# Performance work log

Measured on AMD Instinct MI355X. Metric: run time of the kernel, lower is better.

Reference implementation:

```python
import jax, jax.numpy as jnp
import numpy as np

N = 100000
E = 1600000
IN_C, HID_C, OUT_C = 32, 64, 32


def setup_inputs() -> dict:
    key = jax.random.key(0)
    ks = jax.random.split(key, 10)
    x = jax.random.normal(ks[0], (N, IN_C), dtype=jnp.float32)
    edge_index = jax.random.randint(ks[1], (2, E), 0, N, dtype=jnp.int64)

    def lin(k, fan_in, fan_out):
        kw, kb = jax.random.split(k)
        bound = 1.0 / np.sqrt(fan_in)
        W = jax.random.uniform(kw, (fan_in, fan_out), minval=-bound, maxval=bound, dtype=jnp.float32)
        b = jax.random.uniform(kb, (fan_out,), minval=-bound, maxval=bound, dtype=jnp.float32)
        return W, b

    W1, b1 = lin(ks[2], IN_C, HID_C)
    W2, b2 = lin(ks[3], HID_C, HID_C)
    W3, b3 = lin(ks[4], HID_C, HID_C)
    W4, b4 = lin(ks[5], HID_C, OUT_C)
    return {"x": x, "edge_index": edge_index,
            "W1": W1, "b1": b1, "W2": W2, "b2": b2,
            "W3": W3, "b3": b3, "W4": W4, "b4": b4}


def _gin_conv(x, src, dst, W_a, b_a, W_b, b_b):
    # sum-aggregate neighbor features: messages x[src] scattered to dst
    agg = jax.ops.segment_sum(x[src], dst, num_segments=N)  # [N, d]
    h = agg + x  # (1 + eps) * x with eps = 0
    h = jax.nn.relu(h @ W_a + b_a)
    return h @ W_b + b_b


def reference(x, edge_index, W1, b1, W2, b2, W3, b3, W4, b4):
    src, dst = edge_index[0], edge_index[1]
    h = jax.nn.relu(_gin_conv(x, src, dst, W1, b1, W2, b2))
    out = _gin_conv(h, src, dst, W3, b3, W4, b4)
    return out
```

## Files before the change

kernel.cpp:

```cpp
#include <hip/hip_runtime.h>
#include <hip/hip_fp16.h>

#define NN 100000
#define NE 1600000
#define NB 391
#define NS 13
#define NSP1 14
#define SLICE_SHIFT 13
#define NSEG 391
#define EPB 4096
#define GRID_E 391

typedef _Float16 h2_t __attribute__((ext_vector_type(2)));

__device__ __forceinline__ unsigned pkh2(float lo, float hi) {
    auto v = __builtin_amdgcn_cvt_pkrtz(lo, hi);
    unsigned u; __builtin_memcpy(&u, &v, 4); return u;
}
__device__ __forceinline__ float fdot2u(unsigned a, unsigned b, float c) {
    h2_t x, y; __builtin_memcpy(&x, &a, 4); __builtin_memcpy(&y, &b, 4);
    return __builtin_amdgcn_fdot2(x, y, c, false);
}

__device__ __forceinline__ void h4acc(float2 raw, float& ax, float& ay, float& az, float& aw) {
    __half2 lo = *reinterpret_cast<__half2*>(&raw.x);
    __half2 hi = *reinterpret_cast<__half2*>(&raw.y);
    float2 a = __half22float2(lo);
    float2 b = __half22float2(hi);
    ax += a.x; ay += a.y; az += b.x; aw += b.y;
}


__global__ __launch_bounds__(256) void seghist_k(const int* __restrict__ ei,
                                                 int* __restrict__ segcnt) {
    __shared__ int cnt[NSEG];
    for (int i = threadIdx.x; i < NSEG; i += 256) cnt[i] = 0;
    __syncthreads();
    int eb = blockIdx.x * EPB;
    int ee = (eb + EPB < NE) ? eb + EPB : NE;
    for (int e = eb + threadIdx.x; e < ee; e += 256)
        atomicAdd(&cnt[ei[NE + e] >> 8], 1);
    __syncthreads();
    for (int i = threadIdx.x; i < NSEG; i += 256)
        if (cnt[i]) atomicAdd(&segcnt[i], cnt[i]);
}

__global__ __launch_bounds__(512) void segscan_k(const int* __restrict__ segcnt,
                                                 int* __restrict__ segstart,
                                                 int* __restrict__ cursorA) {
    __shared__ int tmp[512];
    int t = threadIdx.x;
    int v = (t < NSEG) ? segcnt[t] : 0;
    tmp[t] = v;
    __syncthreads();
#pragma unroll
    for (int off = 1; off < 512; off <<= 1) {
        int u = (t >= off) ? tmp[t - off] : 0;
        __syncthreads();
        tmp[t] += u;
        __syncthreads();
    }
    if (t < NSEG) {
        int excl = tmp[t] - v;
        segstart[t] = excl;
        cursorA[t] = excl;
    }
    if (t == 0) segstart[NSEG] = NE;
}

__global__ __launch_bounds__(256) void fillA_k(const int* __restrict__ ei,
                                               int* __restrict__ cursorA,
                                               int* __restrict__ segbuf) {
    __shared__ int cnt[NSEG];
    __shared__ int base[NSEG];
    for (int i = threadIdx.x; i < NSEG; i += 256) cnt[i] = 0;
    __syncthreads();

    int eb = blockIdx.x * EPB;
    int pay[16], sb[16];
#pragma unroll
    for (int k = 0; k < 16; ++k) {
        int e = eb + k * 256 + threadIdx.x;
        sb[k] = -1;
        pay[k] = 0;
        if (e < NE) {
            int src = ei[e];
            int dst = ei[NE + e];
            int seg = dst >> 8;
            int off = atomicAdd(&cnt[seg], 1);
            pay[k] = ((dst & 255) << 17) | src;
            sb[k] = (seg << 12) | off;
        }
    }
    __syncthreads();
    for (int b = threadIdx.x; b < NSEG; b += 256)
        base[b] = cnt[b] ? atomicAdd(&cursorA[b], cnt[b]) : 0;
    __syncthreads();
#pragma unroll
    for (int k = 0; k < 16; ++k) {
        if (sb[k] >= 0) {
            int seg = sb[k] >> 12;
            int off = sb[k] & 4095;
            segbuf[base[seg] + off] = pay[k];
        }
    }
}


__global__ __launch_bounds__(256) void deghist_k(const int* __restrict__ segbuf,
                                                 const int* __restrict__ segstart,
                                                 int* __restrict__ deg2) {
    __shared__ int cnt[256 * NS];
    for (int i = threadIdx.x; i < 256 * NS; i += 256) cnt[i] = 0;
    __syncthreads();
    int s0 = segstart[blockIdx.x], s1 = segstart[blockIdx.x + 1];
    for (int e = s0 + threadIdx.x; e < s1; e += 256) {
        int pk = segbuf[e];
        int l = pk >> 17;
        int src = pk & 0x1FFFF;
        atomicAdd(&cnt[l * NS + (src >> SLICE_SHIFT)], 1);
    }
    __syncthreads();
    int n = blockIdx.x * 256 + threadIdx.x;
    if (n < NN) {
#pragma unroll
        for (int s = 0; s < NS; ++s)
            deg2[n * NS + s] = cnt[threadIdx.x * NS + s];
    }
}

__global__ __launch_bounds__(256) void scan1_k(const int* __restrict__ deg2,
                                               int* __restrict__ scanned,
                                               int* __restrict__ bsums) {
    __shared__ int tmp[256];
    int i = blockIdx.x * 256 + threadIdx.x;
    int v = 0;
    if (i < NN) {
#pragma unroll
        for (int k = 0; k < NS; ++k) v += deg2[i * NS + k];
    }
    tmp[threadIdx.x] = v;
    __syncthreads();
#pragma unroll
    for (int off = 1; off < 256; off <<= 1) {
        int t = (threadIdx.x >= off) ? tmp[threadIdx.x - off] : 0;
        __syncthreads();
        tmp[threadIdx.x] += t;
        __syncthreads();
    }
    if (i < NN) scanned[i] = tmp[threadIdx.x];
    if (threadIdx.x == 255) bsums[blockIdx.x] = tmp[255];
}

__global__ __launch_bounds__(512) void scan2_k(int* __restrict__ bsums) {
    __shared__ int tmp[512];
    int v = (threadIdx.x < NB) ? bsums[threadIdx.x] : 0;
    tmp[threadIdx.x] = v;
    __syncthreads();
#pragma unroll
    for (int off = 1; off < 512; off <<= 1) {
        int t = (threadIdx.x >= off) ? tmp[threadIdx.x - off] : 0;
        __syncthreads();
        tmp[threadIdx.x] += t;
        __syncthreads();
    }
    if (threadIdx.x < NB) bsums[threadIdx.x] = tmp[threadIdx.x];
}

__global__ __launch_bounds__(256) void scan3b_k(const int* __restrict__ scanned,
                                                const int* __restrict__ bsums,
                                                const int* __restrict__ deg2,
                                                int* __restrict__ P) {
    int i = blockIdx.x * 256 + threadIdx.x;
    if (i < NN) {
        int d = 0;
#pragma unroll
        for (int k = 0; k < NS; ++k) d += deg2[i * NS + k];
        int incl = scanned[i] + (blockIdx.x ? bsums[blockIdx.x - 1] : 0);
        int run = incl - d;
        P[i * NSP1 + 0] = run;
#pragma unroll
        for (int s = 0; s < NS; ++s) {
            P[i * NSP1 + s + 1] = run;
            run += deg2[i * NS + s];
        }
        if (i == NN - 1) P[NN * NSP1] = incl;
    }
}

__global__ __launch_bounds__(256) void fillB_k(const int* __restrict__ segbuf,
                                               const int* __restrict__ segstart,
                                               const int* __restrict__ P,
                                               int* __restrict__ col) {
    __shared__ int cur[256 * NS];
    int n = blockIdx.x * 256 + threadIdx.x;
    if (n < NN) {
#pragma unroll
        for (int s = 0; s < NS; ++s)
            cur[threadIdx.x * NS + s] = P[n * NSP1 + s + 1];
    }
    __syncthreads();
    int s0 = segstart[blockIdx.x], s1 = segstart[blockIdx.x + 1];
    for (int e = s0 + threadIdx.x; e < s1; e += 256) {
        int pk = segbuf[e];
        int l = pk >> 17;
        int src = pk & 0x1FFFF;
        int pos = atomicAdd(&cur[l * NS + (src >> SLICE_SHIFT)], 1);
        col[pos] = src;
    }
}

__global__ __launch_bounds__(256) void cvtpack_k(const float2* __restrict__ x2,
                                                 __half2* __restrict__ x16,
                                                 const float* __restrict__ W1,
                                                 const float* __restrict__ W2,
                                                 const float* __restrict__ W3,
                                                 const float* __restrict__ W4,
                                                 unsigned* __restrict__ W1p,
                                                 unsigned* __restrict__ W2p,
                                                 unsigned* __restrict__ W3p,
                                                 unsigned* __restrict__ W4p) {
    int i = blockIdx.x * 256 + threadIdx.x;
    if (i < NN * 16) {
        float2 v = x2[i];
        x16[i] = __floats2half2_rn(v.x, v.y);
    }
    if (i < 16 * 64) {
        int p = i >> 6, j = i & 63;
        W1p[i] = pkh2(W1[(2 * p) * 64 + j], W1[(2 * p + 1) * 64 + j]);
    }
    if (i < 32 * 64) {
        int p = i >> 6, j = i & 63;
        W2p[i] = pkh2(W2[(2 * p) * 64 + j], W2[(2 * p + 1) * 64 + j]);
        W3p[i] = pkh2(W3[(2 * p) * 64 + j], W3[(2 * p + 1) * 64 + j]);
    }
    if (i < 32 * 32) {
        int p = i >> 5, j = i & 31;
        W4p[i] = pkh2(W4[(2 * p) * 32 + j], W4[(2 * p + 1) * 32 + j]);
    }
}

__global__ __launch_bounds__(256) void fused1(const float* __restrict__ x,
                                              const float2* __restrict__ x16f2,
                                              const int* __restrict__ P,
                                              const int* __restrict__ col,
                                              const unsigned* __restrict__ W1p,
                                              const float* __restrict__ b1,
                                              const unsigned* __restrict__ W2p,
                                              const float* __restrict__ b2,
                                              __half* __restrict__ h16) {
    __shared__ unsigned W1s[16 * 64];
    __shared__ unsigned W2s[32 * 64];
    __shared__ float b1s[64];
    __shared__ float b2s[64];
    __shared__ unsigned aggL[4][16];
    __shared__ unsigned tL[4][32];
    for (int i = threadIdx.x; i < 16 * 64; i += 256) W1s[i] = W1p[i];
    for (int i = threadIdx.x; i < 32 * 64; i += 256) W2s[i] = W2p[i];
    if (threadIdx.x < 64) {
        b1s[threadIdx.x] = b1[threadIdx.x];
        b2s[threadIdx.x] = b2[threadIdx.x];
    }
    __syncthreads();

    int lane = threadIdx.x & 63;
    int cq = lane & 7;
    int g = lane >> 3;
    int wv = threadIdx.x >> 6;
    int gw = blockIdx.x * 4 + wv;
    int nwaves = gridDim.x * 4;

    int node = gw;
    int s0 = (node < NN) ? P[node * NSP1] : 0;
    int s1 = (node < NN) ? P[(node + 1) * NSP1] : 0;
    while (node < NN) {
        int nnode = node + nwaves;
        int s0n = (nnode < NN) ? P[nnode * NSP1] : 0;
        int s1n = (nnode < NN) ? P[(nnode + 1) * NSP1] : 0;

        float4 sf = ((const float4*)x)[(size_t)node * 8 + cq];

        float ax0 = 0.f, ay0 = 0.f, az0 = 0.f, aw0 = 0.f;
        float ax1 = 0.f, ay1 = 0.f, az1 = 0.f, aw1 = 0.f;
        int e = s0;
        for (; e + 15 < s1; e += 16) {
            int c0 = col[e + g];
            int c1 = col[e + 8 + g];
            float2 f0 = x16f2[(size_t)c0 * 8 + cq];
            float2 f1 = x16f2[(size_t)c1 * 8 + cq];
            h4acc(f0, ax0, ay0, az0, aw0);
            h4acc(f1, ax1, ay1, az1, aw1);
        }
        for (int ee = e + g; ee < s1; ee += 8) {
            float2 f = x16f2[(size_t)col[ee] * 8 + cq];
            h4acc(f, ax0, ay0, az0, aw0);
        }
        float avx = ax0 + ax1, avy = ay0 + ay1, avz = az0 + az1, avw = aw0 + aw1;
        avx += __shfl_xor(avx, 8);  avy += __shfl_xor(avy, 8);
        avz += __shfl_xor(avz, 8);  avw += __shfl_xor(avw, 8);
        avx += __shfl_xor(avx, 16); avy += __shfl_xor(avy, 16);
        avz += __shfl_xor(avz, 16); avw += __shfl_xor(avw, 16);
        avx += __shfl_xor(avx, 32); avy += __shfl_xor(avy, 32);
        avz += __shfl_xor(avz, 32); avw += __shfl_xor(avw, 32);
        avx += sf.x; avy += sf.y; avz += sf.z; avw += sf.w;

        unsigned u0 = pkh2(avx, avy);
        unsigned u1 = pkh2(avz, avw);
        if (lane < 8)
            *reinterpret_cast<uint2*>(&aggL[wv][2 * cq]) = make_uint2(u0, u1);

        float sa = b1s[lane], sb = 0.f;
#pragma unroll
        for (int i = 0; i < 8; ++i) {
            uint2 A = *reinterpret_cast<const uint2*>(&aggL[wv][2 * i]);
            sa = fdot2u(A.x, W1s[(2 * i) * 64 + lane],     sa);
            sb = fdot2u(A.y, W1s[(2 * i + 1) * 64 + lane], sb);
        }
        float t = fmaxf(sa + sb, 0.f);

        float tt = __shfl_xor(t, 1);
        unsigned tp = pkh2((lane & 1) ? tt : t, (lane & 1) ? t : tt);
        if (!(lane & 1)) tL[wv][lane >> 1] = tp;

        float oa = b2s[lane], ob = 0.f;
#pragma unroll
        for (int q = 0; q < 32; q += 2) {
            uint2 T = *reinterpret_cast<const uint2*>(&tL[wv][q]);
            oa = fdot2u(T.x, W2s[q * 64 + lane],       oa);
            ob = fdot2u(T.y, W2s[(q + 1) * 64 + lane], ob);
        }
        h16[(size_t)node * 64 + lane] = __float2half(fmaxf(oa + ob, 0.f));

        node = nnode; s0 = s0n; s1 = s1n;
    }
}

__global__ __launch_bounds__(256) void fused2(const float2* __restrict__ hf2,
                                              const int* __restrict__ P,
                                              const int* __restrict__ col,
                                              const unsigned* __restrict__ W3p,
                                              const float* __restrict__ b3,
                                              const unsigned* __restrict__ W4p,
                                              const float* __restrict__ b4,
                                              float* __restrict__ out) {
    __shared__ unsigned W3s[32 * 64];
    __shared__ unsigned W4s[32 * 32];
    __shared__ float b3s[64];
    __shared__ float b4s[32];
    __shared__ unsigned aggL[4][32];
    __shared__ unsigned tL[4][32];
    for (int i = threadIdx.x; i < 32 * 64; i += 256) W3s[i] = W3p[i];
    for (int i = threadIdx.x; i < 32 * 32; i += 256) W4s[i] = W4p[i];
    if (threadIdx.x < 64) b3s[threadIdx.x] = b3[threadIdx.x];
    if (threadIdx.x < 32) b4s[threadIdx.x] = b4[threadIdx.x];
    __syncthreads();

    int lane = threadIdx.x & 63;
    int cq = lane & 15;
    int g = lane >> 4;
    int wv = threadIdx.x >> 6;
    int gw = blockIdx.x * 4 + wv;
    int nwaves = gridDim.x * 4;

    int node = gw;
    int s0 = (node < NN) ? P[node * NSP1] : 0;
    int s1 = (node < NN) ? P[(node + 1) * NSP1] : 0;
    while (node < NN) {
        int nnode = node + nwaves;
        int s0n = (nnode < NN) ? P[nnode * NSP1] : 0;
        int s1n = (nnode < NN) ? P[(nnode + 1) * NSP1] : 0;

        float2 sfr = hf2[(size_t)node * 16 + cq];

        float ax0 = 0.f, ay0 = 0.f, az0 = 0.f, aw0 = 0.f;
        float ax1 = 0.f, ay1 = 0.f, az1 = 0.f, aw1 = 0.f;
        float ax2 = 0.f, ay2 = 0.f, az2 = 0.f, aw2 = 0.f;
        float ax3 = 0.f, ay3 = 0.f, az3 = 0.f, aw3 = 0.f;
        int e = s0;
        for (; e + 15 < s1; e += 16) {
            int c0 = col[e + g];
            int c1 = col[e + 4 + g];
            int c2 = col[e + 8 + g];
            int c3 = col[e + 12 + g];
            float2 f0 = hf2[(size_t)c0 * 16 + cq];
            float2 f1 = hf2[(size_t)c1 * 16 + cq];
            float2 f2 = hf2[(size_t)c2 * 16 + cq];
            float2 f3 = hf2[(size_t)c3 * 16 + cq];
            h4acc(f0, ax0, ay0, az0, aw0);
            h4acc(f1, ax1, ay1, az1, aw1);
            h4acc(f2, ax2, ay2, az2, aw2);
            h4acc(f3, ax3, ay3, az3, aw3);
        }
        for (int ee = e + g; ee < s1; ee += 4) {
            float2 f = hf2[(size_t)col[ee] * 16 + cq];
            h4acc(f, ax0, ay0, az0, aw0);
        }
        float avx = (ax0 + ax1) + (ax2 + ax3);
        float avy = (ay0 + ay1) + (ay2 + ay3);
        float avz = (az0 + az1) + (az2 + az3);
        float avw = (aw0 + aw1) + (aw2 + aw3);
        avx += __shfl_xor(avx, 16); avy += __shfl_xor(avy, 16);
        avz += __shfl_xor(avz, 16); avw += __shfl_xor(avw, 16);
        avx += __shfl_xor(avx, 32); avy += __shfl_xor(avy, 32);
        avz += __shfl_xor(avz, 32); avw += __shfl_xor(avw, 32);
        {
            __half2 lo = *reinterpret_cast<__half2*>(&sfr.x);
            __half2 hi = *reinterpret_cast<__half2*>(&sfr.y);
            float2 a = __half22float2(lo), b = __half22float2(hi);
            avx += a.x; avy += a.y; avz += b.x; avw += b.y;
        }

        unsigned u0 = pkh2(avx, avy);
        unsigned u1 = pkh2(avz, avw);
        if (lane < 16)
            *reinterpret_cast<uint2*>(&aggL[wv][2 * cq]) = make_uint2(u0, u1);

        float sa = b3s[lane], sb = 0.f;
#pragma unroll
        for (int i = 0; i < 16; ++i) {
            uint2 A = *reinterpret_cast<const uint2*>(&aggL[wv][2 * i]);
            sa = fdot2u(A.x, W3s[(2 * i) * 64 + lane],     sa);
            sb = fdot2u(A.y, W3s[(2 * i + 1) * 64 + lane], sb);
        }
        float t = fmaxf(sa + sb, 0.f);

        float tt = __shfl_xor(t, 1);
        unsigned tp = pkh2((lane & 1) ? tt : t, (lane & 1) ? t : tt);
        if (!(lane & 1)) tL[wv][lane >> 1] = tp;

        float oa = b4s[lane & 31], ob = 0.f;
#pragma unroll
        for (int q = 0; q < 32; q += 2) {
            uint2 T = *reinterpret_cast<const uint2*>(&tL[wv][q]);
            oa = fdot2u(T.x, W4s[q * 32 + (lane & 31)],       oa);
            ob = fdot2u(T.y, W4s[(q + 1) * 32 + (lane & 31)], ob);
        }
        if (lane < 32) out[(size_t)node * 32 + lane] = oa + ob;

        node = nnode; s0 = s0n; s1 = s1n;
    }
}

extern "C" void kernel_launch(void* const* d_in, const int* in_sizes, int n_in,
                              void* d_out, int out_size, void* d_ws, size_t ws_size,
                              hipStream_t stream) {
    const float* x  = (const float*)d_in[0];
    const int*   ei = (const int*)d_in[1];
    const float* W1 = (const float*)d_in[2];
    const float* b1 = (const float*)d_in[3];
    const float* W2 = (const float*)d_in[4];
    const float* b2 = (const float*)d_in[5];
    const float* W3 = (const float*)d_in[6];
    const float* b3 = (const float*)d_in[7];
    const float* W4 = (const float*)d_in[8];
    const float* b4 = (const float*)d_in[9];
    float* out = (float*)d_out;

    char* ws = (char*)d_ws;
    __half* h16   = (__half*)ws;                      ws += (size_t)NN * 64 * 2;
    __half* x16   = (__half*)ws;                      ws += (size_t)NN * 32 * 2;
    int*   col    = (int*)ws;                         ws += (size_t)NE * 4;
    int*   P      = (int*)ws;                         ws += (size_t)(NN * NSP1 + 1) * 4;
    int*   deg2   = (int*)ws;                         ws += (size_t)NN * NS * 4;
    int*   segbuf = (int*)ws;                         ws += (size_t)NE * 4;
    int* scanned  = (int*)ws;                         ws += (size_t)NN * 4;
    int*   bsums  = (int*)ws;                         ws += (size_t)NB * 4;
    int*  segcnt  = (int*)ws;                         ws += (size_t)NSEG * 4;
    int* segstart = (int*)ws;                         ws += (size_t)(NSEG + 1) * 4;
    int* cursorA  = (int*)ws;                         ws += (size_t)NSEG * 4;
    unsigned* W1p = (unsigned*)ws;                    ws += (size_t)16 * 64 * 4;
    unsigned* W2p = (unsigned*)ws;                    ws += (size_t)32 * 64 * 4;
    unsigned* W3p = (unsigned*)ws;                    ws += (size_t)32 * 64 * 4;
    unsigned* W4p = (unsigned*)ws;                    ws += (size_t)32 * 32 * 4;

    (void)hipMemsetAsync(segcnt, 0, (size_t)NSEG * 4, stream);
    cvtpack_k<<<(NN * 16 + 255) / 256, 256, 0, stream>>>((const float2*)x, (__half2*)x16,
                                                         W1, W2, W3, W4, W1p, W2p, W3p, W4p);
    seghist_k<<<GRID_E, 256, 0, stream>>>(ei, segcnt);
    segscan_k<<<1, 512, 0, stream>>>(segcnt, segstart, cursorA);
    fillA_k<<<GRID_E, 256, 0, stream>>>(ei, cursorA, segbuf);
    deghist_k<<<NSEG, 256, 0, stream>>>(segbuf, segstart, deg2);
    scan1_k<<<NB, 256, 0, stream>>>(deg2, scanned, bsums);
    scan2_k<<<1, 512, 0, stream>>>(bsums);
    scan3b_k<<<NB, 256, 0, stream>>>(scanned, bsums, deg2, P);
    fillB_k<<<NSEG, 256, 0, stream>>>(segbuf, segstart, P, col);

    fused1<<<2048, 256, 0, stream>>>(x, (const float2*)x16, P, col,
                                     W1p, b1, W2p, b2, h16);
    fused2<<<2048, 256, 0, stream>>>((const float2*)h16, P, col,
                                     W3p, b3, W4p, b4, out);
}
```

Measured before the change: 232.3 us.

## Prefetch next node's first neighbor indices and widen CSR-build slices

In both fused GIN kernels, each wave now loads the first 16 column indices of the next node during the current node's work. The first gather chunk can then issue without waiting on a dependent col[] load, which hides part of the index-load latency in the pointer-chasing gather. Separately, the partition slice constants change (fewer, larger slices: NS 13→7, SLICE_SHIFT 13→14), which alters the CSR-build bucketing and the P stride. The prefetch costs a few extra registers per wave.

```diff
diff --git a/kernel.cpp b/kernel.cpp
--- a/kernel.cpp
+++ b/kernel.cpp
@@ -4,9 +4,9 @@
 #define NN 100000
 #define NE 1600000
 #define NB 391
-#define NS 13
-#define NSP1 14
-#define SLICE_SHIFT 13
+#define NS 7
+#define NSP1 8
+#define SLICE_SHIFT 14
 #define NSEG 391
 #define EPB 4096
 #define GRID_E 391
@@ -273,23 +273,37 @@
     int node = gw;
     int s0 = (node < NN) ? P[node * NSP1] : 0;
     int s1 = (node < NN) ? P[(node + 1) * NSP1] : 0;
+    bool full = (node < NN) && (s0 + 15 < s1);
+    int pc0 = 0, pc1 = 0;
+    if (full) { pc0 = col[s0 + g]; pc1 = col[s0 + 8 + g]; }
+
     while (node < NN) {
         int nnode = node + nwaves;
         int s0n = (nnode < NN) ? P[nnode * NSP1] : 0;
         int s1n = (nnode < NN) ? P[(nnode + 1) * NSP1] : 0;
+        bool fulln = (nnode < NN) && (s0n + 15 < s1n);
+        int nc0 = 0, nc1 = 0;
+        if (fulln) { nc0 = col[s0n + g]; nc1 = col[s0n + 8 + g]; }
 
         float4 sf = ((const float4*)x)[(size_t)node * 8 + cq];
 
         float ax0 = 0.f, ay0 = 0.f, az0 = 0.f, aw0 = 0.f;
         float ax1 = 0.f, ay1 = 0.f, az1 = 0.f, aw1 = 0.f;
         int e = s0;
-        for (; e + 15 < s1; e += 16) {
-            int c0 = col[e + g];
-            int c1 = col[e + 8 + g];
-            float2 f0 = x16f2[(size_t)c0 * 8 + cq];
-            float2 f1 = x16f2[(size_t)c1 * 8 + cq];
+        if (full) {
+            float2 f0 = x16f2[(size_t)pc0 * 8 + cq];
+            float2 f1 = x16f2[(size_t)pc1 * 8 + cq];
             h4acc(f0, ax0, ay0, az0, aw0);
             h4acc(f1, ax1, ay1, az1, aw1);
+            e = s0 + 16;
+            for (; e + 15 < s1; e += 16) {
+                int c0 = col[e + g];
+                int c1 = col[e + 8 + g];
+                float2 g0 = x16f2[(size_t)c0 * 8 + cq];
+                float2 g1 = x16f2[(size_t)c1 * 8 + cq];
+                h4acc(g0, ax0, ay0, az0, aw0);
+                h4acc(g1, ax1, ay1, az1, aw1);
+            }
         }
         for (int ee = e + g; ee < s1; ee += 8) {
             float2 f = x16f2[(size_t)col[ee] * 8 + cq];
@@ -331,7 +345,7 @@
         }
         h16[(size_t)node * 64 + lane] = __float2half(fmaxf(oa + ob, 0.f));
 
-        node = nnode; s0 = s0n; s1 = s1n;
+        node = nnode; s0 = s0n; s1 = s1n; full = fulln; pc0 = nc0; pc1 = nc1;
     }
 }
 
@@ -365,10 +379,23 @@
     int node = gw;
     int s0 = (node < NN) ? P[node * NSP1] : 0;
     int s1 = (node < NN) ? P[(node + 1) * NSP1] : 0;
+    bool full = (node < NN) && (s0 + 15 < s1);
+    int pc0 = 0, pc1 = 0, pc2 = 0, pc3 = 0;
+    if (full) {
+        pc0 = col[s0 + g];     pc1 = col[s0 + 4 + g];
+        pc2 = col[s0 + 8 + g]; pc3 = col[s0 + 12 + g];
+    }
+
     while (node < NN) {
         int nnode = node + nwaves;
         int s0n = (nnode < NN) ? P[nnode * NSP1] : 0;
         int s1n = (nnode < NN) ? P[(nnode + 1) * NSP1] : 0;
+        bool fulln = (nnode < NN) && (s0n + 15 < s1n);
+        int nc0 = 0, nc1 = 0, nc2 = 0, nc3 = 0;
+        if (fulln) {
+            nc0 = col[s0n + g];     nc1 = col[s0n + 4 + g];
+            nc2 = col[s0n + 8 + g]; nc3 = col[s0n + 12 + g];
+        }
 
         float2 sfr = hf2[(size_t)node * 16 + cq];
 
@@ -377,19 +404,30 @@
         float ax2 = 0.f, ay2 = 0.f, az2 = 0.f, aw2 = 0.f;
         float ax3 = 0.f, ay3 = 0.f, az3 = 0.f, aw3 = 0.f;
         int e = s0;
-        for (; e + 15 < s1; e += 16) {
-            int c0 = col[e + g];
-            int c1 = col[e + 4 + g];
-            int c2 = col[e + 8 + g];
-            int c3 = col[e + 12 + g];
-            float2 f0 = hf2[(size_t)c0 * 16 + cq];
-            float2 f1 = hf2[(size_t)c1 * 16 + cq];
-            float2 f2 = hf2[(size_t)c2 * 16 + cq];
-            float2 f3 = hf2[(size_t)c3 * 16 + cq];
+        if (full) {
+            float2 f0 = hf2[(size_t)pc0 * 16 + cq];
+            float2 f1 = hf2[(size_t)pc1 * 16 + cq];
+            float2 f2 = hf2[(size_t)pc2 * 16 + cq];
+            float2 f3 = hf2[(size_t)pc3 * 16 + cq];
             h4acc(f0, ax0, ay0, az0, aw0);
             h4acc(f1, ax1, ay1, az1, aw1);
             h4acc(f2, ax2, ay2, az2, aw2);
             h4acc(f3, ax3, ay3, az3, aw3);
+            e = s0 + 16;
+            for (; e + 15 < s1; e += 16) {
+                int c0 = col[e + g];
+                int c1 = col[e + 4 + g];
+                int c2 = col[e + 8 + g];
+                int c3 = col[e + 12 + g];
+                float2 g0 = hf2[(size_t)c0 * 16 + cq];
+                float2 g1 = hf2[(size_t)c1 * 16 + cq];
+                float2 g2 = hf2[(size_t)c2 * 16 + cq];
+                float2 g3 = hf2[(size_t)c3 * 16 + cq];
+                h4acc(g0, ax0, ay0, az0, aw0);
+                h4acc(g1, ax1, ay1, az1, aw1);
+                h4acc(g2, ax2, ay2, az2, aw2);
+                h4acc(g3, ax3, ay3, az3, aw3);
+            }
         }
         for (int ee = e + g; ee < s1; ee += 4) {
             float2 f = hf2[(size_t)col[ee] * 16 + cq];
@@ -437,7 +475,8 @@
         }
         if (lane < 32) out[(size_t)node * 32 + lane] = oa + ob;
 
-        node = nnode; s0 = s0n; s1 = s1n;
+        node = nnode; s0 = s0n; s1 = s1n; full = fulln;
+        pc0 = nc0; pc1 = nc1; pc2 = nc2; pc3 = nc3;
     }
 }
 
```

Result: faster. 225.9 us (-2.7%).
